# Optimization experiments

Hardware: AMD Instinct MI355X
Metric: run time of the kernel (lower is better)

The kernel has to match this reference:

```python
import jax, jax.numpy as jnp
import numpy as np

B, T, LBL = 256, 1024, 128  # batch, seq_len, label_size (incl. start/end)
NUM = LBL - 2               # real emission labels


def setup_inputs() -> dict:
    key = jax.random.key(0)
    k1, k2, k3, k4 = jax.random.split(key, 4)
    logits = jax.random.normal(k1, (B, T, NUM), jnp.float32)
    labels = jax.random.randint(k2, (B, T), 0, NUM)
    lens = jax.random.randint(k3, (B,), 1, T + 1)  # 1..T inclusive
    transition = jax.random.normal(k4, (LBL, LBL), jnp.float32)
    # CRF.initialize(): nothing may transition INTO start-row source or OUT of end
    transition = transition.at[:, LBL - 1].set(-100.0)
    transition = transition.at[LBL - 2, :].set(-100.0)
    return {"logits": logits, "labels": labels, "lens": lens, "transition": transition}


def reference(logits, labels, lens, transition):
    """CRF negative-free log-likelihood pieces: returns gold_score - norm_score per sequence ([B])."""
    Bb, Tt, num = logits.shape
    L = transition.shape[0]
    start, end = L - 2, L - 1

    # pad_logits: append two -1000 columns for start/end labels -> [B, T, L]
    pads = jnp.full((Bb, Tt, 2), -1000.0, logits.dtype)
    lg = jnp.concatenate([logits, pads], axis=2)

    # ---- gold unary score ----
    mask_t = jnp.arange(Tt)[None, :] < lens[:, None]            # [B, T]
    unary = jnp.take_along_axis(lg, labels[..., None], axis=2)[..., 0]
    unary = jnp.where(mask_t, unary, 0.0).sum(axis=1)

    # ---- gold binary (transition) score ----
    ext = jnp.concatenate(
        [jnp.full((Bb, 1), start, labels.dtype), labels,
         jnp.full((Bb, 1), end, labels.dtype)], axis=1)          # [B, T+2]
    mask_e = jnp.arange(Tt + 2)[None, :] < (lens + 1)[:, None]
    ext = jnp.where(mask_e, ext, end)                            # positions >= len+1 -> end
    trn_scr = transition[ext[:, 1:], ext[:, :-1]]                # [B, T+1] (row=next, col=prev)
    mask_b = jnp.arange(Tt + 1)[None, :] < (lens + 1)[:, None]
    binary = jnp.where(mask_b, trn_scr, 0.0).sum(axis=1)

    gold = unary + binary

    # ---- partition (norm) score via log-sum-exp scan over time ----
    alpha0 = jnp.full((Bb, L), -100.0, lg.dtype).at[:, start].set(0.0)
    lg_t = jnp.transpose(lg, (1, 0, 2))                          # [T, B, L]

    def step(alpha, xs):
        logit, t = xs                                            # logit: [B, L]
        # mat[b, j, i] = logit[b, j] + alpha[b, i] + transition[j, i]
        mat = logit[:, :, None] + alpha[:, None, :] + transition[None]
        alpha_nxt = jax.nn.logsumexp(mat, axis=2)                # [B, L]
        alpha = jnp.where((t < lens)[:, None], alpha_nxt, alpha)
        return alpha, None

    alpha, _ = jax.lax.scan(step, alpha0, (lg_t, jnp.arange(Tt)))
    alpha = alpha + transition[end][None, :]
    norm = jax.nn.logsumexp(alpha, axis=1)                       # [B]

    return gold - norm
```

## Files before the change

### kernel.cpp

```cpp
#include <hip/hip_runtime.h>


typedef _Float16 half_t;
typedef _Float16 h2 __attribute__((ext_vector_type(2)));
typedef _Float16 h8 __attribute__((ext_vector_type(8)));

#define TB  1024
#define NUM 126
#define LBL 128

__device__ __forceinline__ float dot2f(h2 a, h2 b, float c) {
  return __builtin_amdgcn_fdot2(a, b, c, false);
}

template <int U>
__device__ __forceinline__ float dotu(h8 a, h8 e, float c) {
  return dot2f(__builtin_shufflevector(a, a, 2 * U, 2 * U + 1),
               __builtin_shufflevector(e, e, 2 * U, 2 * U + 1), c);
}

template <int CTRL>
__device__ __forceinline__ float dpp_max_step(float x) {
  int xi = __float_as_int(x);
  int yi = __builtin_amdgcn_update_dpp(xi, xi, CTRL, 0xF, 0xF, false);
  return fmaxf(x, __int_as_float(yi));
}

__device__ __forceinline__ float wave_max_tree(float x) {
  x = dpp_max_step<0x111>(x);
  x = dpp_max_step<0x112>(x);
  x = dpp_max_step<0x114>(x);
  x = dpp_max_step<0x118>(x);
  x = dpp_max_step<0x142>(x);
  x = dpp_max_step<0x143>(x);
  return x;
}

__device__ __forceinline__ float wave_max64(float x) {
  return __int_as_float(
      __builtin_amdgcn_readlane(__float_as_int(wave_max_tree(x)), 63));
}

__device__ __forceinline__ float half_sum(float x) {
  int a = __float_as_int(x), b = __float_as_int(x);
  asm("v_permlane32_swap_b32 %0, %1" : "+v"(a), "+v"(b));
  return __int_as_float(a) + __int_as_float(b);
}

__global__ __launch_bounds__(256, 1)
void crf_fwd(const float* __restrict__ logits, const int* __restrict__ labels,
             const int* __restrict__ lens, const float* __restrict__ trans,
             float* __restrict__ out)
{
  const int b    = blockIdx.x;
  const int tid  = threadIdx.x;
  const int wid  = tid >> 6;
  const int l    = tid & 63;
  const int half = l >> 5;
  const int r    = (wid << 5) + (l & 31);
  const int rr   = (r < NUM) ? r : (NUM - 1);
  const float rmask = (r < NUM) ? 1.0f : 0.0f;
  const int len  = lens[b];

  __shared__ __align__(16) h2    a_sh[2][64];
  __shared__ __align__(16) float maxsh[2][4];
  __shared__ float goldsh[4], Msh[4], psh[4];

  const float* lgbase = logits + (size_t)b * TB * NUM;
  const int*   lab    = labels + (size_t)b * TB;

  h8 E[8];
  {
    const float* tr = trans + r * LBL + half * 64;
    #pragma unroll
    for (int q = 0; q < 8; ++q) {
      h8 v;
      #pragma unroll
      for (int e = 0; e < 8; ++e) v[e] = (half_t)__expf(tr[8 * q + e]);
      E[q] = v;
    }
  }

  float g = 0.f;
  #pragma unroll
  for (int kk = 0; kk < 4; ++kk) {
    int t = tid + 256 * kk;
    if (t < len) {
      int lt = lab[t];
      int lp = (t == 0) ? (LBL - 2) : lab[t - 1];
      g += lgbase[(size_t)t * NUM + lt] + trans[lt * LBL + lp];
    }
  }
  if (tid == 0) g += trans[(LBL - 1) * LBL + lab[len - 1]];
  #pragma unroll
  for (int o = 1; o < 64; o <<= 1) g += __shfl_xor(g, o);
  if (l == 0) goldsh[wid] = g;

  if (tid < 64) {
    h2 ai;
    ai[0] = (half_t)((2 * tid     == LBL - 2) ? 1.0f : 0.0f);
    ai[1] = (half_t)((2 * tid + 1 == LBL - 2) ? 1.0f : 0.0f);
    a_sh[0][tid] = ai;
  }
  if (tid < 8) maxsh[tid >> 2][tid & 3] = 64.0f;
  __syncthreads();

  float plg[4];
  #pragma unroll
  for (int d = 0; d < 4; ++d) plg[d] = lgbase[(size_t)d * NUM + rr];

  int P = 6, Kacc = 0, Kout = 0, par = 0;
  float w_out = 1.f;

#define STEP_BODY(Q)                                                        \
  {                                                                         \
       \
    const float4 mv = *(const float4*)(&maxsh[par][0]);                     \
    const h8* ap = (const h8*)(&a_sh[par][0]) + half * 8;                   \
    float eL = __expf(Q) * rmask;                                           \
    float s0 = 0.f, s1 = 0.f, s2 = 0.f, s3 = 0.f;                           \
    _Pragma("unroll")                                                       \
    for (int q = 0; q < 8; q += 2) {                                        \
      h8 avA = ap[q], avB = ap[q + 1];                                      \
      h8 eA = E[q], eB = E[q + 1];                                          \
      s0 = dotu<0>(avA, eA, s0);  s1 = dotu<1>(avA, eA, s1);                \
      s2 = dotu<2>(avA, eA, s2);  s3 = dotu<3>(avA, eA, s3);                \
      s0 = dotu<0>(avB, eB, s0);  s1 = dotu<1>(avB, eB, s1);                \
      s2 = dotu<2>(avB, eB, s2);  s3 = dotu<3>(avB, eB, s3);                \
    }                                                                       \
    float mm = fmaxf(fmaxf(mv.x, mv.y), fmaxf(mv.z, mv.w));                 \
    P = (((__float_as_int(mm) >> 23) & 0xFF) - 127) - P + 6;                \
         \
    float ssum = half_sum((s0 + s1) + (s2 + s3));                           \
    float w = ssum * eL;                                                    \
    float sc = __int_as_float((127 - P) << 23);            \
    ((half_t*)(&a_sh[par ^ 1][0]))[r] = (half_t)(w * sc);    \
    Kout = Kacc;  Kacc += P;                           \
    float m = wave_max_tree(w);                                             \
    if (l == 63) maxsh[par ^ 1][wid] = m;                                   \
            \
    asm volatile("s_waitcnt lgkmcnt(0)\n\ts_barrier" ::: "memory");         \
    w_out = w;  par ^= 1;                                                   \
  }

  int t = 0;
  for (; t + 4 <= len; t += 4) {
    int q0 = t + 4, q1 = t + 5, q2 = t + 6, q3 = t + 7;
    q0 = (q0 < TB) ? q0 : (TB - 1);  q1 = (q1 < TB) ? q1 : (TB - 1);
    q2 = (q2 < TB) ? q2 : (TB - 1);  q3 = (q3 < TB) ? q3 : (TB - 1);
    STEP_BODY(plg[0])
    plg[0] = lgbase[(size_t)q0 * NUM + rr];
    STEP_BODY(plg[1])
    plg[1] = lgbase[(size_t)q1 * NUM + rr];
    STEP_BODY(plg[2])
    plg[2] = lgbase[(size_t)q2 * NUM + rr];
    STEP_BODY(plg[3])
    plg[3] = lgbase[(size_t)q3 * NUM + rr];
  }
  const int rem = len - t;
  if (rem > 0) STEP_BODY(plg[0])
  if (rem > 1) STEP_BODY(plg[1])
  if (rem > 2) STEP_BODY(plg[2])
#undef STEP_BODY

  const float LN2 = 0.6931471805599453f;
  float v = (float)Kout * LN2 + __logf(w_out) + trans[(LBL - 1) * LBL + r];
  if (half) v = -__builtin_inff();
  float M = wave_max64(v);
  float p = __expf(v - M);
  #pragma unroll
  for (int o = 1; o < 64; o <<= 1) p += __shfl_xor(p, o);
  if (l == 0) { Msh[wid] = M; psh[wid] = p; }
  __syncthreads();
  if (tid == 0) {
    float gT = goldsh[0] + goldsh[1] + goldsh[2] + goldsh[3];
    float Mg = fmaxf(fmaxf(Msh[0], Msh[1]), fmaxf(Msh[2], Msh[3]));
    float pg = psh[0] * __expf(Msh[0] - Mg) + psh[1] * __expf(Msh[1] - Mg)
             + psh[2] * __expf(Msh[2] - Mg) + psh[3] * __expf(Msh[3] - Mg);
    out[b] = gT - (Mg + __logf(pg));
  }
}

extern "C" void kernel_launch(void* const* d_in, const int* in_sizes, int n_in,
                              void* d_out, int out_size, void* d_ws, size_t ws_size,
                              hipStream_t stream) {
  const float* logits = (const float*)d_in[0];
  const int*   labels = (const int*)d_in[1];
  const int*   lens   = (const int*)d_in[2];
  const float* trans  = (const float*)d_in[3];
  float* out = (float*)d_out;
  (void)in_sizes; (void)n_in; (void)out_size; (void)d_ws; (void)ws_size;
  crf_fwd<<<256, 256, 0, stream>>>(logits, labels, lens, trans, out);
}
```

Measured before the change: 485.5 us.

## Remap lanes to two output rows by quarter-K split with DPP quad reduction

Each lane now computes two output labels over a quarter of the source dimension, instead of one label over half of it. Each alpha vector read from shared memory is reused for two rows, and the cross-lane reduction becomes two DPP add steps in place of a permlane32 swap. Logit loads become float2 and a single packed h2 store per row pair. This aims to cut LDS reads per step and shorten the serial critical path. In exchange it adds a second reduction chain and leaves only one lane in four doing the store.

```diff
diff --git a/kernel.cpp b/kernel.cpp
--- a/kernel.cpp
+++ b/kernel.cpp
@@ -41,10 +41,17 @@
       __builtin_amdgcn_readlane(__float_as_int(wave_max_tree(x)), 63));
 }
 
-__device__ __forceinline__ float half_sum(float x) {
-  int a = __float_as_int(x), b = __float_as_int(x);
-  asm("v_permlane32_swap_b32 %0, %1" : "+v"(a), "+v"(b));
-  return __int_as_float(a) + __int_as_float(b);
+template <int CTRL>
+__device__ __forceinline__ float dpp_add_step(float x) {
+  int xi = __float_as_int(x);
+  int yi = __builtin_amdgcn_update_dpp(xi, xi, CTRL, 0xF, 0xF, false);
+  return x + __int_as_float(yi);
+}
+
+__device__ __forceinline__ float quad_sum(float x) {
+  x = dpp_add_step<0xB1>(x);
+  x = dpp_add_step<0x4E>(x);
+  return x;
 }
 
 __global__ __launch_bounds__(256, 1)
@@ -52,15 +59,18 @@
              const int* __restrict__ lens, const float* __restrict__ trans,
              float* __restrict__ out)
 {
-  const int b    = blockIdx.x;
-  const int tid  = threadIdx.x;
-  const int wid  = tid >> 6;
-  const int l    = tid & 63;
-  const int half = l >> 5;
-  const int r    = (wid << 5) + (l & 31);
-  const int rr   = (r < NUM) ? r : (NUM - 1);
-  const float rmask = (r < NUM) ? 1.0f : 0.0f;
-  const int len  = lens[b];
+  const int b   = blockIdx.x;
+  const int tid = threadIdx.x;
+  const int wid = tid >> 6;
+  const int l   = tid & 63;
+  const int q   = l & 3;
+  const int p   = l >> 2;
+  const int r0  = (wid << 5) + (p << 1);
+  const int r1  = r0 + 1;
+  const float rm0 = (r0 < NUM) ? 1.0f : 0.0f;
+  const float rm1 = (r1 < NUM) ? 1.0f : 0.0f;
+  const int rre = (r0 < NUM - 1) ? r0 : (NUM - 2);
+  const int len = lens[b];
 
   __shared__ __align__(16) h2    a_sh[2][64];
   __shared__ __align__(16) float maxsh[2][4];
@@ -69,15 +79,19 @@
   const float* lgbase = logits + (size_t)b * TB * NUM;
   const int*   lab    = labels + (size_t)b * TB;
 
-  h8 E[8];
+  h8 E0[4], E1[4];
   {
-    const float* tr = trans + r * LBL + half * 64;
+    const float* t0 = trans + r0 * LBL + q * 32;
+    const float* t1 = trans + r1 * LBL + q * 32;
     #pragma unroll
-    for (int q = 0; q < 8; ++q) {
-      h8 v;
+    for (int c = 0; c < 4; ++c) {
+      h8 v0, v1;
       #pragma unroll
-      for (int e = 0; e < 8; ++e) v[e] = (half_t)__expf(tr[8 * q + e]);
-      E[q] = v;
+      for (int e = 0; e < 8; ++e) {
+        v0[e] = (half_t)__expf(t0[8 * c + e]);
+        v1[e] = (half_t)__expf(t1[8 * c + e]);
+      }
+      E0[c] = v0; E1[c] = v1;
     }
   }
 
@@ -105,42 +119,45 @@
   if (tid < 8) maxsh[tid >> 2][tid & 3] = 64.0f;
   __syncthreads();
 
-  float plg[4];
-  #pragma unroll
-  for (int d = 0; d < 4; ++d) plg[d] = lgbase[(size_t)d * NUM + rr];
+  float2 plg[4];
+  #pragma unroll
+  for (int d = 0; d < 4; ++d)
+    plg[d] = *(const float2*)(lgbase + (size_t)d * NUM + rre);
 
   int P = 6, Kacc = 0, Kout = 0, par = 0;
-  float w_out = 1.f;
-
-#define STEP_BODY(Q)                                                        \
-  {                                                                         \
-       \
-    const float4 mv = *(const float4*)(&maxsh[par][0]);                     \
-    const h8* ap = (const h8*)(&a_sh[par][0]) + half * 8;                   \
-    float eL = __expf(Q) * rmask;                                           \
-    float s0 = 0.f, s1 = 0.f, s2 = 0.f, s3 = 0.f;                           \
-    _Pragma("unroll")                                                       \
-    for (int q = 0; q < 8; q += 2) {                                        \
-      h8 avA = ap[q], avB = ap[q + 1];                                      \
-      h8 eA = E[q], eB = E[q + 1];                                          \
-      s0 = dotu<0>(avA, eA, s0);  s1 = dotu<1>(avA, eA, s1);                \
-      s2 = dotu<2>(avA, eA, s2);  s3 = dotu<3>(avA, eA, s3);                \
-      s0 = dotu<0>(avB, eB, s0);  s1 = dotu<1>(avB, eB, s1);                \
-      s2 = dotu<2>(avB, eB, s2);  s3 = dotu<3>(avB, eB, s3);                \
-    }                                                                       \
-    float mm = fmaxf(fmaxf(mv.x, mv.y), fmaxf(mv.z, mv.w));                 \
-    P = (((__float_as_int(mm) >> 23) & 0xFF) - 127) - P + 6;                \
-         \
-    float ssum = half_sum((s0 + s1) + (s2 + s3));                           \
-    float w = ssum * eL;                                                    \
-    float sc = __int_as_float((127 - P) << 23);            \
-    ((half_t*)(&a_sh[par ^ 1][0]))[r] = (half_t)(w * sc);    \
-    Kout = Kacc;  Kacc += P;                           \
-    float m = wave_max_tree(w);                                             \
-    if (l == 63) maxsh[par ^ 1][wid] = m;                                   \
-            \
-    asm volatile("s_waitcnt lgkmcnt(0)\n\ts_barrier" ::: "memory");         \
-    w_out = w;  par ^= 1;                                                   \
+  float w0_out = 1.f, w1_out = 1.f;
+
+#define DOT8(acc, av, ev)                                                   \
+    acc = dotu<0>(av, ev, acc); acc = dotu<1>(av, ev, acc);                 \
+    acc = dotu<2>(av, ev, acc); acc = dotu<3>(av, ev, acc);
+
+#define STEP_BODY(Qv)                                                      \
+  {                                                                        \
+    const float4 mv = *(const float4*)(&maxsh[par][0]);                    \
+    const h8* ap = (const h8*)(&a_sh[par][0]) + q * 4;                     \
+    float eL0 = __expf((Qv).x) * rm0;                                      \
+    float eL1 = __expf((Qv).y) * rm1;                                      \
+    h8 av0 = ap[0], av1 = ap[1], av2 = ap[2], av3 = ap[3];                 \
+    float sA = 0.f, sB = 0.f, sC = 0.f, sD = 0.f;                          \
+    DOT8(sA, av0, E0[0])  DOT8(sC, av0, E1[0])                             \
+    DOT8(sA, av1, E0[1])  DOT8(sC, av1, E1[1])                             \
+    DOT8(sB, av2, E0[2])  DOT8(sD, av2, E1[2])                             \
+    DOT8(sB, av3, E0[3])  DOT8(sD, av3, E1[3])                             \
+    float mm = fmaxf(fmaxf(mv.x, mv.y), fmaxf(mv.z, mv.w));                \
+    P = (((__float_as_int(mm) >> 23) & 0xFF) - 127) - P + 6;               \
+    float w0 = quad_sum(sA + sB) * eL0;                                    \
+    float w1 = quad_sum(sC + sD) * eL1;                                    \
+    float sc = __int_as_float((127 - P) << 23);           \
+    h2 pk;                                                                 \
+    pk[0] = (half_t)(w0 * sc);                                             \
+    pk[1] = (half_t)(w1 * sc);                                             \
+    if (q == 0) a_sh[par ^ 1][(wid << 4) + p] = pk;                        \
+    Kout = Kacc;  Kacc += P;                          \
+    float m = wave_max_tree(fmaxf(w0, w1));                                \
+    if (l == 63) maxsh[par ^ 1][wid] = m;                                  \
+           \
+    asm volatile("s_waitcnt lgkmcnt(0)\n\ts_barrier" ::: "memory");        \
+    w0_out = w0;  w1_out = w1;  par ^= 1;                                  \
   }
 
   int t = 0;
@@ -149,28 +166,31 @@
     q0 = (q0 < TB) ? q0 : (TB - 1);  q1 = (q1 < TB) ? q1 : (TB - 1);
     q2 = (q2 < TB) ? q2 : (TB - 1);  q3 = (q3 < TB) ? q3 : (TB - 1);
     STEP_BODY(plg[0])
-    plg[0] = lgbase[(size_t)q0 * NUM + rr];
+    plg[0] = *(const float2*)(lgbase + (size_t)q0 * NUM + rre);
     STEP_BODY(plg[1])
-    plg[1] = lgbase[(size_t)q1 * NUM + rr];
+    plg[1] = *(const float2*)(lgbase + (size_t)q1 * NUM + rre);
     STEP_BODY(plg[2])
-    plg[2] = lgbase[(size_t)q2 * NUM + rr];
+    plg[2] = *(const float2*)(lgbase + (size_t)q2 * NUM + rre);
     STEP_BODY(plg[3])
-    plg[3] = lgbase[(size_t)q3 * NUM + rr];
+    plg[3] = *(const float2*)(lgbase + (size_t)q3 * NUM + rre);
   }
   const int rem = len - t;
   if (rem > 0) STEP_BODY(plg[0])
   if (rem > 1) STEP_BODY(plg[1])
   if (rem > 2) STEP_BODY(plg[2])
 #undef STEP_BODY
+#undef DOT8
 
   const float LN2 = 0.6931471805599453f;
-  float v = (float)Kout * LN2 + __logf(w_out) + trans[(LBL - 1) * LBL + r];
-  if (half) v = -__builtin_inff();
-  float M = wave_max64(v);
-  float p = __expf(v - M);
-  #pragma unroll
-  for (int o = 1; o < 64; o <<= 1) p += __shfl_xor(p, o);
-  if (l == 0) { Msh[wid] = M; psh[wid] = p; }
+  float K = (float)Kout * LN2;
+  float v0 = K + __logf(w0_out) + trans[(LBL - 1) * LBL + r0];
+  float v1 = K + __logf(w1_out) + trans[(LBL - 1) * LBL + r1];
+  if (q != 0) { v0 = -__builtin_inff(); v1 = -__builtin_inff(); }
+  float M = wave_max64(fmaxf(v0, v1));
+  float pp = __expf(v0 - M) + __expf(v1 - M);
+  #pragma unroll
+  for (int o = 1; o < 64; o <<= 1) pp += __shfl_xor(pp, o);
+  if (l == 0) { Msh[wid] = M; psh[wid] = pp; }
   __syncthreads();
   if (tid == 0) {
     float gT = goldsh[0] + goldsh[1] + goldsh[2] + goldsh[3];
```

After: 482.1 us. Within noise of the previous version (-0.7%).
